# Optimization experiments

Measured on AMD Instinct MI355X. Metric: run time of the kernel, lower is better.

The kernel has to match this reference:

```python
import jax, jax.numpy as jnp
import numpy as np

B, S, E = 4, 2048, 1024
H, D = 16, 64  # num_heads, head_size; H*D == E


def setup_inputs() -> dict:
    key = jax.random.key(0)
    ks = jax.random.split(key, 6)
    scale = E ** -0.5
    x = jax.random.normal(ks[0], (B, S, E), dtype=jnp.float32)
    # per-head bias-free q/k/v projections, stacked over heads: [H, E, D]
    Wq = jax.random.normal(ks[1], (H, E, D), dtype=jnp.float32) * scale
    Wk = jax.random.normal(ks[2], (H, E, D), dtype=jnp.float32) * scale
    Wv = jax.random.normal(ks[3], (H, E, D), dtype=jnp.float32) * scale
    # output projection: Linear(H*D, E) with bias
    Wproj = jax.random.normal(ks[4], (H * D, E), dtype=jnp.float32) * ((H * D) ** -0.5)
    bproj = jax.random.normal(ks[5], (E,), dtype=jnp.float32) * 0.01
    return {"x": x, "Wq": Wq, "Wk": Wk, "Wv": Wv, "Wproj": Wproj, "bproj": bproj}


def reference(x, Wq, Wk, Wv, Wproj, bproj):
    # Batched equivalent of the per-head loop: each head h computes
    # q = x @ Wq[h], k = x @ Wk[h], v = x @ Wv[h]
    q = jnp.einsum("bse,hed->bhsd", x, Wq)
    k = jnp.einsum("bse,hed->bhsd", x, Wk)
    v = jnp.einsum("bse,hed->bhsd", x, Wv)
    # causal scaled dot-product attention, scale = head_size**-0.5
    scores = jnp.einsum("bhqd,bhkd->bhqk", q, k) * (D ** -0.5)
    causal = jnp.tril(jnp.ones((S, S), dtype=bool))  # [S, S]
    scores = jnp.where(causal, scores, jnp.finfo(scores.dtype).min)
    attn = jax.nn.softmax(scores, axis=-1)  # dropout = identity in eval
    out = jnp.einsum("bhqk,bhkd->bhqd", attn, v)
    # concat heads along the feature dim, then project (dropout = identity)
    out = out.transpose(0, 2, 1, 3).reshape(B, S, H * D)
    return out @ Wproj + bproj
```

## Files before the change

### kernel.cpp

```cpp
#include <hip/hip_runtime.h>
#include <stdint.h>

typedef unsigned short u16;
typedef __attribute__((ext_vector_type(8))) short bf16x8;
typedef __attribute__((ext_vector_type(4))) float f32x4;

#define S_LEN 2048
#define EDIM 1024
#define NH 16
#define HD 64

static __device__ __forceinline__ u16 f2bf(float f) {
  union { float f; uint32_t u; } v; v.f = f;
  uint32_t r = v.u + 0x7fffu + ((v.u >> 16) & 1u);
  return (u16)(r >> 16);
}

static __device__ __forceinline__ void gload_lds16(const u16* g, u16* l) {
  __builtin_amdgcn_global_load_lds(
      (const __attribute__((address_space(1))) void*)g,
      (__attribute__((address_space(3))) void*)l, 16, 0, 0);
}

static __device__ __forceinline__ bf16x8 gload16(const u16* p) {
  bf16x8 r;
  asm volatile("global_load_dwordx4 %0, %1, off" : "=v"(r) : "v"(p));
  return r;
}

#define WAIT_VM(n)                                   \
  do {                                               \
    asm volatile("s_waitcnt vmcnt(" #n ")");         \
    __builtin_amdgcn_sched_barrier(0);               \
  } while (0)

#define BARRIER()                                    \
  do {                                               \
    __builtin_amdgcn_s_barrier();                    \
    __builtin_amdgcn_sched_barrier(0);               \
  } while (0)

__global__ __launch_bounds__(256) void pack_inputs(
    const float* __restrict__ x, const float* __restrict__ Wq,
    const float* __restrict__ Wk, const float* __restrict__ Wv,
    const float* __restrict__ Wp,
    u16* __restrict__ xb, u16* __restrict__ wqkvT, u16* __restrict__ wprojT) {
  int idx = blockIdx.x * 256 + threadIdx.x;
  const int n_x4 = (4 * S_LEN * EDIM) / 4;
  const int n_qkv = 3 * NH * HD * EDIM;
  if (idx < n_x4) {
    float4 v = ((const float4*)x)[idx];
    ushort4 o;
    o.x = f2bf(v.x); o.y = f2bf(v.y); o.z = f2bf(v.z); o.w = f2bf(v.w);
    ((ushort4*)xb)[idx] = o;
  } else if (idx < n_x4 + n_qkv) {
    int i = idx - n_x4;
    int c = i >> 10;
    int e = i & 1023;
    int m = c >> 10;
    int rem = c & 1023;
    int h = rem >> 6;
    int d = rem & 63;
    const float* W = (m == 0) ? Wq : (m == 1) ? Wk : Wv;
    wqkvT[i] = f2bf(W[(h * EDIM + e) * HD + d]);
  } else {
    int j = idx - n_x4 - n_qkv;
    if (j < EDIM * EDIM) {
      int n = j >> 10, k = j & 1023;
      wprojT[j] = f2bf(Wp[k * EDIM + n]);
    }
  }
}

template <int EPI>
__global__ __launch_bounds__(256) void gemm128(
    const u16* __restrict__ A, const u16* __restrict__ Bt,
    const float* __restrict__ bias,
    u16* __restrict__ o0, u16* __restrict__ o1, u16* __restrict__ o2,
    float* __restrict__ of, int K, int N) {
  __shared__ __align__(16) u16 As[128 * 32];
  __shared__ __align__(16) u16 Bs[128 * 32];
  const int tid  = threadIdx.x;
  const int lane = tid & 63;
  const int wave = tid >> 6;
  const int wm = wave >> 1;
  const int wn = wave & 1;
  const int col = lane & 15;
  const int quad = lane >> 4;
  const int m0 = blockIdx.y << 7;
  const int n0 = blockIdx.x << 7;

  const int srow = (wave << 5) + (lane >> 2);
  const int scol = (lane & 3) << 3;
  const u16* gA = A + (size_t)(m0 + srow) * K + scol;
  const u16* gB = Bt + (size_t)(n0 + srow) * K + scol;
  u16* lA = &As[(wave << 5) << 5];
  u16* lB = &Bs[(wave << 5) << 5];

  f32x4 acc[4][4];
#pragma unroll
  for (int i = 0; i < 4; i++)
#pragma unroll
    for (int j = 0; j < 4; j++) acc[i][j] = (f32x4){0.f, 0.f, 0.f, 0.f};

  for (int kk = 0; kk < K; kk += 32) {
    __syncthreads();
#pragma unroll
    for (int i = 0; i < 2; i++) {
      gload_lds16(gA + (size_t)(i * 16) * K + kk, lA + i * 512);
      gload_lds16(gB + (size_t)(i * 16) * K + kk, lB + i * 512);
    }
    __syncthreads();

    bf16x8 af[4], bfr[4];
#pragma unroll
    for (int i = 0; i < 4; i++)
      af[i] = *(const bf16x8*)(&As[((wm * 64 + i * 16 + col) << 5) + quad * 8]);
#pragma unroll
    for (int j = 0; j < 4; j++)
      bfr[j] = *(const bf16x8*)(&Bs[((wn * 64 + j * 16 + col) << 5) + quad * 8]);
#pragma unroll
    for (int i = 0; i < 4; i++)
#pragma unroll
      for (int j = 0; j < 4; j++)
        acc[i][j] = __builtin_amdgcn_mfma_f32_16x16x32_bf16(af[i], bfr[j],
                                                            acc[i][j], 0, 0, 0);
  }

#pragma unroll
  for (int i = 0; i < 4; i++) {
#pragma unroll
    for (int j = 0; j < 4; j++) {
      const int rg0 = m0 + wm * 64 + i * 16 + quad * 4;
      const int cg = n0 + wn * 64 + j * 16 + col;
      if (EPI == 0) {
        const int mat = cg >> 10;
        const int rem = cg & 1023;
        const int h = rem >> 6;
        const int d = rem & 63;
        const int b = rg0 >> 11;
        const int s0 = rg0 & 2047;
        if (mat == 2) {
          ushort4 o;
          o.x = f2bf(acc[i][j][0]); o.y = f2bf(acc[i][j][1]);
          o.z = f2bf(acc[i][j][2]); o.w = f2bf(acc[i][j][3]);
          *(ushort4*)(&o2[(((size_t)(b * NH + h) * HD + d) << 11) + s0]) = o;
        } else {
          u16* dst = (mat == 0) ? o0 : o1;
#pragma unroll
          for (int r = 0; r < 4; r++)
            dst[((size_t)((b * NH + h) * S_LEN + s0 + r) << 6) + d] =
                f2bf(acc[i][j][r]);
        }
      } else {
#pragma unroll
        for (int r = 0; r < 4; r++)
          of[(size_t)(rg0 + r) * N + cg] = acc[i][j][r] + bias[cg];
      }
    }
  }
}

__global__ __launch_bounds__(256, 3) void attn_fused(
    const u16* __restrict__ Q, const u16* __restrict__ K,
    const u16* __restrict__ Vt, u16* __restrict__ O) {
  __shared__ __align__(16) u16 Kbuf[2][64 * 64];
  __shared__ __align__(16) u16 Vbuf[2][64 * 64];
  __shared__ __align__(16) u16 Ps[4][2][16 * 72];

  const int tid  = threadIdx.x;
  const int lane = tid & 63;
  const int wave = tid >> 6;
  const int col  = lane & 15;
  const int quad = lane >> 4;
  const int gid  = blockIdx.x;
  const int bh = ((gid & 7) << 3) | ((gid >> 3) & 7);
  const int qb = 15 - (gid >> 6);
  const int b = bh >> 4;
  const int h = bh & 15;
  const int q0w = qb * 128 + wave * 32;

  const u16* Kbh = K + (size_t)bh * S_LEN * HD;
  const u16* Vbh = Vt + (size_t)bh * HD * S_LEN;

  const int srow  = lane >> 3;
  const int sslot = (lane & 7) ^ srow;
  const int r0a = wave * 16;
  const int r0b = wave * 16 + 8;

  const float C1 = 0.125f * 1.44269504f;
  const float C2 = 8.0f * 1.44269504f;

  bf16x8 qf[2][2];
#pragma unroll
  for (int a = 0; a < 2; a++) {
    const u16* Qrow = Q + ((size_t)bh * S_LEN + q0w + a * 16 + col) * HD;
    qf[a][0] = gload16(Qrow + quad * 8);
    qf[a][1] = gload16(Qrow + 32 + quad * 8);
  }

  f32x4 oacc[2][4];
#pragma unroll
  for (int a = 0; a < 2; a++)
#pragma unroll
    for (int n = 0; n < 4; n++) oacc[a][n] = (f32x4){0.f, 0.f, 0.f, 0.f};
  float lrow[2][4] = {{0.f, 0.f, 0.f, 0.f}, {0.f, 0.f, 0.f, 0.f}};

  auto STAGE = [&](int buf, int kv0) {
    gload_lds16(Kbh + (size_t)(kv0 + r0a + srow) * HD + sslot * 8,
                &Kbuf[buf][r0a * 64]);
    gload_lds16(Kbh + (size_t)(kv0 + r0b + srow) * HD + sslot * 8,
                &Kbuf[buf][r0b * 64]);
    gload_lds16(Vbh + (size_t)(r0a + srow) * S_LEN + kv0 + sslot * 8,
                &Vbuf[buf][r0a * 64]);
    gload_lds16(Vbh + (size_t)(r0b + srow) * S_LEN + kv0 + sslot * 8,
                &Vbuf[buf][r0b * 64]);
  };

  const int T = 2 * qb + 2;
  int cur = 0;
  STAGE(0, 0);
  WAIT_VM(0);
  BARRIER();

  for (int t = 0; t < T; t++) {
    const int kv0 = t << 6;
    if (t + 1 < T) STAGE(cur ^ 1, kv0 + 64);

    if (kv0 <= q0w + 31) {
      f32x4 sc[2][4];
#pragma unroll
      for (int j = 0; j < 4; j++) {
        const u16* kr = &Kbuf[cur][(j * 16 + col) * 64];
        const bf16x8 kf0 = *(const bf16x8*)(kr + ((quad ^ (col & 7)) << 3));
        const bf16x8 kf1 = *(const bf16x8*)(kr + (((4 + quad) ^ (col & 7)) << 3));
#pragma unroll
        for (int a = 0; a < 2; a++) {
          sc[a][j] = (f32x4){0.f, 0.f, 0.f, 0.f};
          sc[a][j] = __builtin_amdgcn_mfma_f32_16x16x32_bf16(qf[a][0], kf0, sc[a][j], 0, 0, 0);
          sc[a][j] = __builtin_amdgcn_mfma_f32_16x16x32_bf16(qf[a][1], kf1, sc[a][j], 0, 0, 0);
        }
      }

      if (kv0 + 63 > q0w) {
#pragma unroll
        for (int a = 0; a < 2; a++)
#pragma unroll
          for (int r = 0; r < 4; r++) {
            const int ql = q0w - kv0 + a * 16 + quad * 4 + r;
#pragma unroll
            for (int j = 0; j < 4; j++) {
              float p = exp2f(sc[a][j][r] * C1 - C2);
              if (j * 16 + col > ql) p = 0.f;
              lrow[a][r] += p;
              Ps[wave][a][(quad * 4 + r) * 72 + j * 16 + col] = f2bf(p);
            }
          }
      } else {
#pragma unroll
        for (int a = 0; a < 2; a++)
#pragma unroll
          for (int r = 0; r < 4; r++)
#pragma unroll
            for (int j = 0; j < 4; j++) {
              const float p = exp2f(sc[a][j][r] * C1 - C2);
              lrow[a][r] += p;
              Ps[wave][a][(quad * 4 + r) * 72 + j * 16 + col] = f2bf(p);
            }
      }
      bf16x8 pf[2][2];
#pragma unroll
      for (int a = 0; a < 2; a++) {
        pf[a][0] = *(const bf16x8*)(&Ps[wave][a][col * 72 + quad * 8]);
        pf[a][1] = *(const bf16x8*)(&Ps[wave][a][col * 72 + 32 + quad * 8]);
      }

#pragma unroll
      for (int n = 0; n < 4; n++) {
        const u16* vr = &Vbuf[cur][(n * 16 + col) * 64];
        const bf16x8 vf0 = *(const bf16x8*)(vr + ((quad ^ (col & 7)) << 3));
        const bf16x8 vf1 = *(const bf16x8*)(vr + (((4 + quad) ^ (col & 7)) << 3));
#pragma unroll
        for (int a = 0; a < 2; a++) {
          oacc[a][n] = __builtin_amdgcn_mfma_f32_16x16x32_bf16(pf[a][0], vf0, oacc[a][n], 0, 0, 0);
          oacc[a][n] = __builtin_amdgcn_mfma_f32_16x16x32_bf16(pf[a][1], vf1, oacc[a][n], 0, 0, 0);
        }
      }
    }

    WAIT_VM(0);
    BARRIER();
    cur ^= 1;
  }

#pragma unroll
  for (int a = 0; a < 2; a++)
#pragma unroll
    for (int r = 0; r < 4; r++) {
      float l = lrow[a][r];
#pragma unroll
      for (int off = 1; off < 16; off <<= 1) l += __shfl_xor(l, off);
      const float inv = 1.0f / l;
      const size_t row = (size_t)b * S_LEN + q0w + a * 16 + quad * 4 + r;
#pragma unroll
      for (int n = 0; n < 4; n++)
        O[row * EDIM + h * HD + n * 16 + col] = f2bf(oacc[a][n][r] * inv);
    }
}

extern "C" void kernel_launch(void* const* d_in, const int* in_sizes, int n_in,
                              void* d_out, int out_size, void* d_ws, size_t ws_size,
                              hipStream_t stream) {
  const float* x  = (const float*)d_in[0];
  const float* Wq = (const float*)d_in[1];
  const float* Wk = (const float*)d_in[2];
  const float* Wv = (const float*)d_in[3];
  const float* Wp = (const float*)d_in[4];
  const float* bp = (const float*)d_in[5];
  float* out = (float*)d_out;

  char* ws = (char*)d_ws;
  u16* wqkvT  = (u16*)(ws);
  u16* wprojT = (u16*)(ws + 6291456);
  u16* Qb     = (u16*)(ws + 8388608);
  u16* Kb     = (u16*)(ws + 25165824);
  u16* Vtb    = (u16*)(ws + 41943040);
  u16* xb     = (u16*)(ws + 58720256);
  u16* Ob     = xb;

  pack_inputs<<<dim3(24576), dim3(256), 0, stream>>>(x, Wq, Wk, Wv, Wp,
                                                     xb, wqkvT, wprojT);
  gemm128<0><<<dim3(24, 64), dim3(256), 0, stream>>>(
      xb, wqkvT, (const float*)nullptr, Qb, Kb, Vtb, (float*)nullptr, 1024, 3072);
  attn_fused<<<dim3(1024), dim3(256), 0, stream>>>(Qb, Kb, Vtb, Ob);
  gemm128<1><<<dim3(8, 64), dim3(256), 0, stream>>>(
      Ob, wprojT, bp, (u16*)nullptr, (u16*)nullptr, (u16*)nullptr, out, 1024, 1024);
}
```

Baseline: 278.0 us.

## Tile weight transposes through LDS and deepen GEMM K-step with XOR swizzle

The weight packing kernel now transposes 64x64 tiles through shared memory, so global reads and bf16 writes are both coalesced; before, each thread converted one strided scalar element. The GEMM kernels now stage 64-wide K slices per barrier pair instead of 32, with an XOR swizzle on the LDS column slot to avoid bank conflicts on fragment reads. This halves the number of synchronisations per K loop but doubles LDS use per block, which may lower occupancy.

```diff
diff --git a/kernel.cpp b/kernel.cpp
--- a/kernel.cpp
+++ b/kernel.cpp
@@ -3,6 +3,7 @@
 
 typedef unsigned short u16;
 typedef __attribute__((ext_vector_type(8))) short bf16x8;
+typedef __attribute__((ext_vector_type(8))) unsigned short u16x8;
 typedef __attribute__((ext_vector_type(4))) float f32x4;
 
 #define S_LEN 2048
@@ -45,29 +46,60 @@
     const float* __restrict__ Wk, const float* __restrict__ Wv,
     const float* __restrict__ Wp,
     u16* __restrict__ xb, u16* __restrict__ wqkvT, u16* __restrict__ wprojT) {
-  int idx = blockIdx.x * 256 + threadIdx.x;
-  const int n_x4 = (4 * S_LEN * EDIM) / 4;
-  const int n_qkv = 3 * NH * HD * EDIM;
-  if (idx < n_x4) {
+  const int blk = blockIdx.x;
+  const int tid = threadIdx.x;
+  if (blk < 8192) {
+    int idx = blk * 256 + tid;
     float4 v = ((const float4*)x)[idx];
     ushort4 o;
     o.x = f2bf(v.x); o.y = f2bf(v.y); o.z = f2bf(v.z); o.w = f2bf(v.w);
     ((ushort4*)xb)[idx] = o;
-  } else if (idx < n_x4 + n_qkv) {
-    int i = idx - n_x4;
-    int c = i >> 10;
-    int e = i & 1023;
-    int m = c >> 10;
-    int rem = c & 1023;
-    int h = rem >> 6;
-    int d = rem & 63;
+    return;
+  }
+  __shared__ u16 tile[64][65];
+  const float* src;
+  size_t src_rs;
+  u16* dst;
+  if (blk < 8960) {
+    int t = blk - 8192;
+    int mh = t >> 4;
+    int et = t & 15;
+    int m = mh >> 4, h = mh & 15;
     const float* W = (m == 0) ? Wq : (m == 1) ? Wk : Wv;
-    wqkvT[i] = f2bf(W[(h * EDIM + e) * HD + d]);
+    src = W + ((size_t)(h * EDIM + et * 64)) * HD;
+    src_rs = HD;
+    dst = wqkvT + (size_t)(m * 1024 + h * 64) * 1024 + et * 64;
   } else {
-    int j = idx - n_x4 - n_qkv;
-    if (j < EDIM * EDIM) {
-      int n = j >> 10, k = j & 1023;
-      wprojT[j] = f2bf(Wp[k * EDIM + n]);
+    int t = blk - 8960;
+    int kt = t >> 4, nt = t & 15;
+    src = Wp + (size_t)(kt * 64) * 1024 + nt * 64;
+    src_rs = 1024;
+    dst = wprojT + (size_t)(nt * 64) * 1024 + kt * 64;
+  }
+  {
+    const int rr = tid >> 4;
+    const int c4 = (tid & 15) << 2;
+#pragma unroll
+    for (int p = 0; p < 4; p++) {
+      const int r = p * 16 + rr;
+      float4 v = *(const float4*)(src + (size_t)r * src_rs + c4);
+      tile[r][c4 + 0] = f2bf(v.x);
+      tile[r][c4 + 1] = f2bf(v.y);
+      tile[r][c4 + 2] = f2bf(v.z);
+      tile[r][c4 + 3] = f2bf(v.w);
+    }
+  }
+  __syncthreads();
+  {
+    const int rr = tid >> 3;
+    const int c8 = (tid & 7) << 3;
+#pragma unroll
+    for (int p = 0; p < 2; p++) {
+      const int r = p * 32 + rr;
+      u16x8 o;
+#pragma unroll
+      for (int j = 0; j < 8; j++) o[j] = tile[c8 + j][r];
+      *(u16x8*)(dst + (size_t)r * 1024 + c8) = o;
     }
   }
 }
@@ -78,8 +110,8 @@
     const float* __restrict__ bias,
     u16* __restrict__ o0, u16* __restrict__ o1, u16* __restrict__ o2,
     float* __restrict__ of, int K, int N) {
-  __shared__ __align__(16) u16 As[128 * 32];
-  __shared__ __align__(16) u16 Bs[128 * 32];
+  __shared__ __align__(16) u16 As[128 * 64];
+  __shared__ __align__(16) u16 Bs[128 * 64];
   const int tid  = threadIdx.x;
   const int lane = tid & 63;
   const int wave = tid >> 6;
@@ -87,15 +119,16 @@
   const int wn = wave & 1;
   const int col = lane & 15;
   const int quad = lane >> 4;
+  const int cs = col & 7;
   const int m0 = blockIdx.y << 7;
   const int n0 = blockIdx.x << 7;
 
-  const int srow = (wave << 5) + (lane >> 2);
-  const int scol = (lane & 3) << 3;
-  const u16* gA = A + (size_t)(m0 + srow) * K + scol;
-  const u16* gB = Bt + (size_t)(n0 + srow) * K + scol;
-  u16* lA = &As[(wave << 5) << 5];
-  u16* lB = &Bs[(wave << 5) << 5];
+  const int srow  = lane >> 3;
+  const int sslot = (lane & 7) ^ srow;
+  const u16* gA = A + (size_t)(m0 + (wave << 5) + srow) * K + sslot * 8;
+  const u16* gB = Bt + (size_t)(n0 + (wave << 5) + srow) * K + sslot * 8;
+  u16* lA = &As[(wave << 5) << 6];
+  u16* lB = &Bs[(wave << 5) << 6];
 
   f32x4 acc[4][4];
 #pragma unroll
@@ -103,28 +136,33 @@
 #pragma unroll
     for (int j = 0; j < 4; j++) acc[i][j] = (f32x4){0.f, 0.f, 0.f, 0.f};
 
-  for (int kk = 0; kk < K; kk += 32) {
+  for (int kk = 0; kk < K; kk += 64) {
     __syncthreads();
 #pragma unroll
-    for (int i = 0; i < 2; i++) {
-      gload_lds16(gA + (size_t)(i * 16) * K + kk, lA + i * 512);
-      gload_lds16(gB + (size_t)(i * 16) * K + kk, lB + i * 512);
+    for (int i = 0; i < 4; i++) {
+      gload_lds16(gA + (size_t)(i * 8) * K + kk, lA + i * 512);
+      gload_lds16(gB + (size_t)(i * 8) * K + kk, lB + i * 512);
     }
     __syncthreads();
 
-    bf16x8 af[4], bfr[4];
-#pragma unroll
-    for (int i = 0; i < 4; i++)
-      af[i] = *(const bf16x8*)(&As[((wm * 64 + i * 16 + col) << 5) + quad * 8]);
-#pragma unroll
-    for (int j = 0; j < 4; j++)
-      bfr[j] = *(const bf16x8*)(&Bs[((wn * 64 + j * 16 + col) << 5) + quad * 8]);
-#pragma unroll
-    for (int i = 0; i < 4; i++)
+#pragma unroll
+    for (int x = 0; x < 2; x++) {
+      bf16x8 af[4], bfr[4];
+#pragma unroll
+      for (int i = 0; i < 4; i++)
+        af[i] = *(const bf16x8*)(
+            &As[((wm * 64 + i * 16 + col) << 6) + ((((x << 2) + quad) ^ cs) << 3)]);
 #pragma unroll
       for (int j = 0; j < 4; j++)
-        acc[i][j] = __builtin_amdgcn_mfma_f32_16x16x32_bf16(af[i], bfr[j],
-                                                            acc[i][j], 0, 0, 0);
+        bfr[j] = *(const bf16x8*)(
+            &Bs[((wn * 64 + j * 16 + col) << 6) + ((((x << 2) + quad) ^ cs) << 3)]);
+#pragma unroll
+      for (int i = 0; i < 4; i++)
+#pragma unroll
+        for (int j = 0; j < 4; j++)
+          acc[i][j] = __builtin_amdgcn_mfma_f32_16x16x32_bf16(af[i], bfr[j],
+                                                              acc[i][j], 0, 0, 0);
+    }
   }
 
 #pragma unroll
@@ -328,8 +366,8 @@
   u16* xb     = (u16*)(ws + 58720256);
   u16* Ob     = xb;
 
-  pack_inputs<<<dim3(24576), dim3(256), 0, stream>>>(x, Wq, Wk, Wv, Wp,
-                                                     xb, wqkvT, wprojT);
+  pack_inputs<<<dim3(9216), dim3(256), 0, stream>>>(x, Wq, Wk, Wv, Wp,
+                                                    xb, wqkvT, wprojT);
   gemm128<0><<<dim3(24, 64), dim3(256), 0, stream>>>(
       xb, wqkvT, (const float*)nullptr, Qb, Kb, Vtb, (float*)nullptr, 1024, 3072);
   attn_fused<<<dim3(1024), dim3(256), 0, stream>>>(Qb, Kb, Vtb, Ob);
```

Result: faster. 261.8 us (-5.8%).
